# Kernel optimization log

Hardware: AMD Instinct MI355X
Metric: run time of the kernel (lower is better)

Reference implementation:

```python
import jax, jax.numpy as jnp
import numpy as np

B, C, H, W = 4, 64, 160, 160
OUT, KH, KW = 64, 3, 3
STRIDE, PAD = 1, 1
K2 = KH * KW


def conv2d(x, w, b=None, stride=STRIDE, pad=PAD):
    y = jax.lax.conv_general_dilated(
        x, w, window_strides=(stride, stride),
        padding=[(pad, pad), (pad, pad)],
        dimension_numbers=("NCHW", "OIHW", "NCHW"))
    if b is not None:
        y = y + b[None, :, None, None]
    return y


def bilinear_gather(x, py, px):
    # x: [B,C,H,W]; py,px: [B,K2,Ho,Wo] float sampling positions
    Bq, Cq, Hq, Wq = x.shape
    y0 = jnp.floor(py)
    x0 = jnp.floor(px)
    wy1 = py - y0  # frac
    wx1 = px - x0
    y0i = y0.astype(jnp.int32)
    x0i = x0.astype(jnp.int32)
    x_flat = x.reshape(Bq, Cq, Hq * Wq)

    def corner(yi, xi, wgt):
        valid = (yi >= 0) & (yi < Hq) & (xi >= 0) & (xi < Wq)
        idx = jnp.clip(yi, 0, Hq - 1) * Wq + jnp.clip(xi, 0, Wq - 1)  # [B,K2,Ho,Wo]
        g = jax.vmap(lambda xf, i: jnp.take(xf, i, axis=1))(x_flat, idx)  # [B,C,K2,Ho,Wo]
        return g * (wgt * valid)[:, None]

    out = corner(y0i, x0i, (1 - wy1) * (1 - wx1))
    out = out + corner(y0i, x0i + 1, (1 - wy1) * wx1)
    out = out + corner(y0i + 1, x0i, wy1 * (1 - wx1))
    out = out + corner(y0i + 1, x0i + 1, wy1 * wx1)
    return out  # [B,C,K2,Ho,Wo]


def deform_forward(x, offset_w, offset_b, mask_w, mask_b, dcn_w):
    offset = conv2d(x, offset_w, offset_b)                # [B, 2*K2, Ho, Wo]
    mask = jax.nn.sigmoid(conv2d(x, mask_w, mask_b))      # [B, K2, Ho, Wo]
    Bq, _, Ho, Wo = offset.shape
    off = offset.reshape(Bq, K2, 2, Ho, Wo)
    off_y, off_x = off[:, :, 0], off[:, :, 1]
    k = jnp.arange(K2)
    ky = (k // KW).astype(jnp.float32)
    kx = (k % KW).astype(jnp.float32)
    base_i = jnp.arange(Ho, dtype=jnp.float32) * STRIDE - PAD
    base_j = jnp.arange(Wo, dtype=jnp.float32) * STRIDE - PAD
    py = off_y + base_i[None, None, :, None] + ky[None, :, None, None]
    px = off_x + base_j[None, None, None, :] + kx[None, :, None, None]
    sampled = bilinear_gather(x, py, px)                  # [B,C,K2,Ho,Wo]
    w = dcn_w.reshape(OUT, C, K2)
    # out[b,o,i,j] = sum_{c,k} w[o,c,k] * mask[b,k,i,j] * sampled[b,c,k,i,j]
    return jnp.einsum("ock,bckij,bkij->boij", w, sampled, mask)


def setup_inputs() -> dict:
    key = jax.random.key(0)
    ks = jax.random.split(key, 6)
    x = jax.random.normal(ks[0], (B, C, H, W), dtype=jnp.float32)
    # small random weights so offsets stay modest (module inits them to 0;
    # random values exercise the full deformable math)
    offset_w = jax.random.normal(ks[1], (2 * K2, C, KH, KW), dtype=jnp.float32) * 0.01
    offset_b = jax.random.normal(ks[2], (2 * K2,), dtype=jnp.float32) * 0.1
    mask_w = jax.random.normal(ks[3], (K2, C, KH, KW), dtype=jnp.float32) * 0.01
    mask_b = jax.random.normal(ks[4], (K2,), dtype=jnp.float32) * 0.1
    dcn_w = jax.random.normal(ks[5], (OUT, C, KH, KW), dtype=jnp.float32) * (1.0 / np.sqrt(C * K2))
    return {"x": x, "offset_w": offset_w, "offset_b": offset_b,
            "mask_w": mask_w, "mask_b": mask_b, "dcn_w": dcn_w}


def reference(x, offset_w, offset_b, mask_w, mask_b, dcn_w):
    return deform_forward(x, offset_w, offset_b, mask_w, mask_b, dcn_w)
```

## Files before the change

kernel.cpp:

```cpp
#include <hip/hip_runtime.h>
#include <math.h>

#define Bq 4
#define Cq 64
#define Hq 160
#define Wq 160
#define HWq (Hq*Wq)
#define OUTq 64
#define KKq 576
#define KS  18
#define SROW 584
#define HSTRIDE 72

typedef __attribute__((ext_vector_type(8))) _Float16 half8;
typedef __attribute__((ext_vector_type(2))) _Float16 half2v;
typedef __attribute__((ext_vector_type(4))) float float4v;
typedef __attribute__((ext_vector_type(4))) unsigned short ushort4v;
typedef unsigned short ushort_t;
typedef unsigned int uint_t;

__device__ __forceinline__ ushort_t f2h(float f) {
    return __builtin_bit_cast(ushort_t, (_Float16)f);
}
__device__ __forceinline__ uint_t f2hdup(float f) {
    uint_t u = (uint_t)f2h(f);
    return u | (u << 16);
}
__device__ __forceinline__ half2v h2(uint_t u) {
    return __builtin_bit_cast(half2v, u);
}
#define MFMA16(a,b,c) __builtin_amdgcn_mfma_f32_16x16x32_f16((a),(b),(c),0,0,0)

__global__ void __launch_bounds__(256) k_prep(const float* __restrict__ x,
                                              const float* __restrict__ dcn_w,
                                              const float* __restrict__ off_w,
                                              const float* __restrict__ msk_w,
                                              ushort_t* __restrict__ xt,
                                              ushort_t* __restrict__ wtf,
                                              ushort_t* __restrict__ cwf2) {
    __shared__ float tile[64][65];
    int b = blockIdx.y, hw0 = blockIdx.x * 64;
    int tid = threadIdx.x;
    int l16 = tid & 15, crow = tid >> 4;
#pragma unroll
    for (int i = 0; i < 4; ++i) {
        int c = crow + i*16;
        float4 v = *(const float4*)(x + ((size_t)(b*Cq + c))*HWq + hw0 + l16*4);
        tile[c][l16*4+0] = v.x;
        tile[c][l16*4+1] = v.y;
        tile[c][l16*4+2] = v.z;
        tile[c][l16*4+3] = v.w;
    }
    __syncthreads();
#pragma unroll
    for (int it = 0; it < 4; ++it) {
        int hw = (tid >> 4) + it*16;
        int c4 = (tid & 15) * 4;
        uint_t v0 = (uint_t)f2h(tile[c4+0][hw]) | ((uint_t)f2h(tile[c4+1][hw]) << 16);
        uint_t v1 = (uint_t)f2h(tile[c4+2][hw]) | ((uint_t)f2h(tile[c4+3][hw]) << 16);
        uint2 vv; vv.x = v0; vv.y = v1;
        *(uint2*)(xt + ((size_t)b*HWq + hw0 + hw)*64 + c4) = vv;
    }
    if (blockIdx.y == 0 && blockIdx.x < 216) {
        int id = blockIdx.x*256 + tid;
        if (id < 4*KS*512) {
            int j = id & 7, ln = (id>>3) & 63, ks = (id>>9) % KS, g = id/(512*KS);
            int kk = ks*32 + (ln>>4)*8 + j;
            int c  = kk & 63, kt = kk >> 6;
            int m  = g*16 + (ln&15);
            wtf[id] = f2h(dcn_w[m*KKq + c*9 + kt]);
        }
        int id2 = id - 4*KS*512;
        if (id2 >= 0 && id2 < 9*2*2*512) {
            int j = id2 & 7, ln = (id2>>3) & 63;
            int ks2 = (id2>>9) & 1, g = (id2>>10) & 1, k = id2 >> 11;
            int co = g*16 + (ln&15);
            int c  = ks2*32 + (ln>>4)*8 + j;
            float w = 0.f;
            if (co < 18)      w = off_w[co*KKq + c*9 + k];
            else if (co < 27) w = msk_w[(co-18)*KKq + c*9 + k];
            cwf2[id2] = f2h(w);
        }
    }
}

__global__ void __launch_bounds__(256, 7) k_fused(const ushort_t* __restrict__ xt,
                                                  const ushort_t* __restrict__ cwf2,
                                                  const float* __restrict__ off_b,
                                                  const float* __restrict__ msk_b,
                                                  const ushort_t* __restrict__ wtf,
                                                  float* __restrict__ out) {
    __shared__ __align__(16) char s_mem[16*SROW*2];
    __shared__ __align__(16) ushort4v s_A16[144];
    __shared__ __align__(16) uint4 s_W[144];
    ushort_t* halo   = (ushort_t*)s_mem;
    float*    s_part = (float*)(s_mem + 7776);
    ushort_t* s_s    = (ushort_t*)s_mem;

    int blk = blockIdx.x;
    int jt = blk % 10, i = (blk/10) % Hq, b = blk/(10*Hq);
    int j0 = jt*16;
    int tid = threadIdx.x, lane = tid & 63, grp = tid >> 6;
    int n = lane & 15, quad = lane >> 4;

    const ushort_t* xtb = xt + (size_t)b*HWq*64;
    for (int t = tid; t < 432; t += 256) {
        int seg = t >> 3, sub = t & 7;
        int ky = seg / 18, px = seg % 18;
        int y = i + ky - 1, xx = j0 + px - 1;
        uint4 v = {0u,0u,0u,0u};
        if (y >= 0 && y < Hq && xx >= 0 && xx < Wq)
            v = *(const uint4*)(xtb + ((size_t)y*Wq + xx)*64 + sub*8);
        *(uint4*)(halo + (ky*18 + px)*HSTRIDE + sub*8) = v;
    }
    __syncthreads();

    {
        int gM = grp & 1, kh = grp >> 1;
        float4v cacc = {0.f,0.f,0.f,0.f};
#pragma unroll
        for (int s = 0; s < 9; ++s) {
            int st = kh*9 + s;
            int k = st >> 1, ks2 = st & 1;
            int ky = k/3, kx = k - (k/3)*3;
            half8 a  = *(const half8*)(cwf2 + (size_t)(((k*2+gM)*2+ks2)*512 + lane*8));
            half8 bf = *(const half8*)(halo + (ky*18 + n + kx)*HSTRIDE + quad*8 + ks2*32);
            cacc = MFMA16(a, bf, cacc);
        }
        *(float4v*)(s_part + grp*256 + lane*4) = cacc;
    }
    __syncthreads();

    if (tid < 144) {
        int p = tid & 15, k = tid >> 4;
        #define RD(co) (s_part[(((co)>>4)*256)     + ((((co)&15)>>2)*16 + p)*4 + ((co)&3)] + \
                        s_part[(2 + ((co)>>4))*256 + ((((co)&15)>>2)*16 + p)*4 + ((co)&3)])
        float oy = RD(2*k)   + off_b[2*k];
        float ox = RD(2*k+1) + off_b[2*k+1];
        float mv = RD(18+k)  + msk_b[k];
        #undef RD
        float m = 1.f/(1.f + __expf(-mv));
        float py = oy + (float)(i - 1 + k/3);
        float px = ox + (float)(j0 + p - 1 + (k - (k/3)*3));
        float fy = floorf(py), fx = floorf(px);
        int y0 = (int)fy, x0 = (int)fx;
        float wy1 = py - fy, wx1 = px - fx;
        float wy0 = 1.f - wy1, wx0 = 1.f - wx1;
        bool vy0 = (y0 >= 0) & (y0 < Hq),   vy1 = (y0+1 >= 0) & (y0+1 < Hq);
        bool vx0 = (x0 >= 0) & (x0 < Wq),   vx1 = (x0+1 >= 0) & (x0+1 < Wq);
        int yc0 = min(max(y0,   0), Hq-1), yc1 = min(max(y0+1, 0), Hq-1);
        int xc0 = min(max(x0,   0), Wq-1), xc1 = min(max(x0+1, 0), Wq-1);
        ushort4v av;
        av.x = (ushort_t)(yc0*Wq + xc0);
        av.y = (ushort_t)(yc0*Wq + xc1);
        av.z = (ushort_t)(yc1*Wq + xc0);
        av.w = (ushort_t)(yc1*Wq + xc1);
        s_A16[tid] = av;
        s_W[tid] = make_uint4(f2hdup((vy0 && vx0) ? wy0*wx0*m : 0.f),
                              f2hdup((vy0 && vx1) ? wy0*wx1*m : 0.f),
                              f2hdup((vy1 && vx0) ? wy1*wx0*m : 0.f),
                              f2hdup((vy1 && vx1) ? wy1*wx1*m : 0.f));
    }
    __syncthreads();

    {
        int lane4 = (lane & 31) * 4;
        int halfi = lane >> 5;
        const char* xtbB = (const char*)xtb;
        char* s_sb = (char*)s_s;
#pragma unroll 2
        for (int iter = 0; iter < 18; ++iter) {
            int t2h = iter*8 + grp*2 + halfi;
            ushort4v A = s_A16[t2h];
            uint4 Wt   = s_W[t2h];
            uint_t dst = (uint_t)((t2h & 15)*(SROW*2) + (t2h >> 4)*128);
            uint_t u00 = *(const uint_t*)(xtbB + (((uint_t)A.x) << 7) + lane4);
            uint_t u01 = *(const uint_t*)(xtbB + (((uint_t)A.y) << 7) + lane4);
            uint_t u10 = *(const uint_t*)(xtbB + (((uint_t)A.z) << 7) + lane4);
            uint_t u11 = *(const uint_t*)(xtbB + (((uint_t)A.w) << 7) + lane4);
            half2v acc2 = h2(u00) * h2(Wt.x);
            acc2 = __builtin_elementwise_fma(h2(u01), h2(Wt.y), acc2);
            acc2 = __builtin_elementwise_fma(h2(u10), h2(Wt.z), acc2);
            acc2 = __builtin_elementwise_fma(h2(u11), h2(Wt.w), acc2);
            *(uint_t*)(s_sb + dst + lane4) = __builtin_bit_cast(uint_t, acc2);
        }
    }
    __syncthreads();

    float4v acc = {0.f,0.f,0.f,0.f};
    const ushort_t* arow = wtf + ((size_t)(grp*KS)*64 + lane)*8;
    const ushort_t* brow = s_s + n*SROW + quad*8;
#pragma unroll
    for (int ks = 0; ks < KS; ++ks) {
        half8 a  = *(const half8*)(arow + ks*512);
        half8 bf = *(const half8*)(brow + ks*32);
        acc = MFMA16(a, bf, acc);
    }

#pragma unroll
    for (int r = 0; r < 4; ++r) {
        int o = grp*16 + quad*4 + r;
        out[(((size_t)b*OUTq + o)*Hq + i)*Wq + j0 + n] = acc[r];
    }
}

extern "C" void kernel_launch(void* const* d_in, const int* in_sizes, int n_in,
                              void* d_out, int out_size, void* d_ws, size_t ws_size,
                              hipStream_t stream) {
    const float* x     = (const float*)d_in[0];
    const float* off_w = (const float*)d_in[1];
    const float* off_b = (const float*)d_in[2];
    const float* msk_w = (const float*)d_in[3];
    const float* msk_b = (const float*)d_in[4];
    const float* dcn_w = (const float*)d_in[5];
    float* out = (float*)d_out;

    char* ws = (char*)d_ws;
    ushort_t* xt   = (ushort_t*)ws;
    ushort_t* wtf  = xt + (size_t)Bq*HWq*64;
    ushort_t* cwf2 = wtf + 4*KS*512;

    hipLaunchKernelGGL(k_prep, dim3(HWq/64, Bq), dim3(256), 0, stream,
                       x, dcn_w, off_w, msk_w, xt, wtf, cwf2);
    hipLaunchKernelGGL(k_fused, dim3(Bq*Hq*10), dim3(256), 0, stream,
                       xt, cwf2, off_b, msk_b, wtf, out);
}
```

Baseline: 133.4 us.

## Widen halo tile and serve bilinear gathers from LDS when in range

The halo loaded into shared memory grows from 3x18 to 5x20 pixels and now has its own buffer instead of sharing space with the sample matrix. The bilinear sampling phase encodes each corner as a halo-relative LDS byte offset when all four corners fall inside the tile. Otherwise it sets a flag bit and falls back to global gathers. This aims to replace most scattered global loads with LDS reads, since offsets are usually small. In exchange, shared memory use grows, the launch-bounds occupancy hint drops from 7 to 4, and half-waves may diverge between the two paths.

```diff
diff --git a/kernel.cpp b/kernel.cpp
--- a/kernel.cpp
+++ b/kernel.cpp
@@ -11,6 +11,9 @@
 #define KS  18
 #define SROW 584
 #define HSTRIDE 72
+#define HROWPX 20
+#define HROWS  5
+#define HALO_B (HROWS*HROWPX*HSTRIDE*2)
 
 typedef __attribute__((ext_vector_type(8))) _Float16 half8;
 typedef __attribute__((ext_vector_type(2))) _Float16 half2v;
@@ -84,18 +87,18 @@
     }
 }
 
-__global__ void __launch_bounds__(256, 7) k_fused(const ushort_t* __restrict__ xt,
+__global__ void __launch_bounds__(256, 4) k_fused(const ushort_t* __restrict__ xt,
                                                   const ushort_t* __restrict__ cwf2,
                                                   const float* __restrict__ off_b,
                                                   const float* __restrict__ msk_b,
                                                   const ushort_t* __restrict__ wtf,
                                                   float* __restrict__ out) {
-    __shared__ __align__(16) char s_mem[16*SROW*2];
+    __shared__ __align__(16) char s_mem[HALO_B + 16*SROW*2];
     __shared__ __align__(16) ushort4v s_A16[144];
     __shared__ __align__(16) uint4 s_W[144];
     ushort_t* halo   = (ushort_t*)s_mem;
-    float*    s_part = (float*)(s_mem + 7776);
-    ushort_t* s_s    = (ushort_t*)s_mem;
+    float*    s_part = (float*)(s_mem + HALO_B);
+    ushort_t* s_s    = (ushort_t*)(s_mem + HALO_B);
 
     int blk = blockIdx.x;
     int jt = blk % 10, i = (blk/10) % Hq, b = blk/(10*Hq);
@@ -104,14 +107,14 @@
     int n = lane & 15, quad = lane >> 4;
 
     const ushort_t* xtb = xt + (size_t)b*HWq*64;
-    for (int t = tid; t < 432; t += 256) {
+    for (int t = tid; t < HROWS*HROWPX*8; t += 256) {
         int seg = t >> 3, sub = t & 7;
-        int ky = seg / 18, px = seg % 18;
-        int y = i + ky - 1, xx = j0 + px - 1;
+        int r = seg / HROWPX, px = seg % HROWPX;
+        int y = i + r - 2, xx = j0 + px - 2;
         uint4 v = {0u,0u,0u,0u};
-        if (y >= 0 && y < Hq && xx >= 0 && xx < Wq)
+        if ((unsigned)y < (unsigned)Hq && (unsigned)xx < (unsigned)Wq)
             v = *(const uint4*)(xtb + ((size_t)y*Wq + xx)*64 + sub*8);
-        *(uint4*)(halo + (ky*18 + px)*HSTRIDE + sub*8) = v;
+        *(uint4*)(halo + (r*HROWPX + px)*HSTRIDE + sub*8) = v;
     }
     __syncthreads();
 
@@ -124,7 +127,7 @@
             int k = st >> 1, ks2 = st & 1;
             int ky = k/3, kx = k - (k/3)*3;
             half8 a  = *(const half8*)(cwf2 + (size_t)(((k*2+gM)*2+ks2)*512 + lane*8));
-            half8 bf = *(const half8*)(halo + (ky*18 + n + kx)*HSTRIDE + quad*8 + ks2*32);
+            half8 bf = *(const half8*)(halo + ((ky+1)*HROWPX + (n + kx + 1))*HSTRIDE + quad*8 + ks2*32);
             cacc = MFMA16(a, bf, cacc);
         }
         *(float4v*)(s_part + grp*256 + lane*4) = cacc;
@@ -151,10 +154,22 @@
         int yc0 = min(max(y0,   0), Hq-1), yc1 = min(max(y0+1, 0), Hq-1);
         int xc0 = min(max(x0,   0), Wq-1), xc1 = min(max(x0+1, 0), Wq-1);
         ushort4v av;
-        av.x = (ushort_t)(yc0*Wq + xc0);
-        av.y = (ushort_t)(yc0*Wq + xc1);
-        av.z = (ushort_t)(yc1*Wq + xc0);
-        av.w = (ushort_t)(yc1*Wq + xc1);
+        bool inh = (yc0 >= i-2) && (yc1 <= i+2) && (xc0 >= j0-2) && (xc1 <= j0+17);
+        if (inh) {
+            int ry0 = (yc0 - (i-2)) * (HROWPX*HSTRIDE*2);
+            int ry1 = (yc1 - (i-2)) * (HROWPX*HSTRIDE*2);
+            int cx0 = (xc0 - (j0-2)) * (HSTRIDE*2);
+            int cx1 = (xc1 - (j0-2)) * (HSTRIDE*2);
+            av.x = (ushort_t)(ry0 + cx0);
+            av.y = (ushort_t)(ry0 + cx1);
+            av.z = (ushort_t)(ry1 + cx0);
+            av.w = (ushort_t)(ry1 + cx1);
+        } else {
+            av.x = (ushort_t)((yc0*Wq + xc0) | 0x8000);
+            av.y = (ushort_t)((yc0*Wq + xc1) | 0x8000);
+            av.z = (ushort_t)((yc1*Wq + xc0) | 0x8000);
+            av.w = (ushort_t)((yc1*Wq + xc1) | 0x8000);
+        }
         s_A16[tid] = av;
         s_W[tid] = make_uint4(f2hdup((vy0 && vx0) ? wy0*wx0*m : 0.f),
                               f2hdup((vy0 && vx1) ? wy0*wx1*m : 0.f),
@@ -167,17 +182,28 @@
         int lane4 = (lane & 31) * 4;
         int halfi = lane >> 5;
         const char* xtbB = (const char*)xtb;
+        const char* haloB = (const char*)s_mem;
         char* s_sb = (char*)s_s;
 #pragma unroll 2
         for (int iter = 0; iter < 18; ++iter) {
             int t2h = iter*8 + grp*2 + halfi;
-            ushort4v A = s_A16[t2h];
-            uint4 Wt   = s_W[t2h];
+            uint2 Ad = *(const uint2*)(&s_A16[t2h]);
+            uint4 Wt = s_W[t2h];
+            uint_t a0 = Ad.x & 0xffffu, a1 = Ad.x >> 16;
+            uint_t a2 = Ad.y & 0xffffu, a3 = Ad.y >> 16;
             uint_t dst = (uint_t)((t2h & 15)*(SROW*2) + (t2h >> 4)*128);
-            uint_t u00 = *(const uint_t*)(xtbB + (((uint_t)A.x) << 7) + lane4);
-            uint_t u01 = *(const uint_t*)(xtbB + (((uint_t)A.y) << 7) + lane4);
-            uint_t u10 = *(const uint_t*)(xtbB + (((uint_t)A.z) << 7) + lane4);
-            uint_t u11 = *(const uint_t*)(xtbB + (((uint_t)A.w) << 7) + lane4);
+            uint_t u00, u01, u10, u11;
+            if (a0 < 0x8000u) {
+                u00 = *(const uint_t*)(haloB + a0 + lane4);
+                u01 = *(const uint_t*)(haloB + a1 + lane4);
+                u10 = *(const uint_t*)(haloB + a2 + lane4);
+                u11 = *(const uint_t*)(haloB + a3 + lane4);
+            } else {
+                u00 = *(const uint_t*)(xtbB + ((a0 & 0x7fffu) << 7) + lane4);
+                u01 = *(const uint_t*)(xtbB + ((a1 & 0x7fffu) << 7) + lane4);
+                u10 = *(const uint_t*)(xtbB + ((a2 & 0x7fffu) << 7) + lane4);
+                u11 = *(const uint_t*)(xtbB + ((a3 & 0x7fffu) << 7) + lane4);
+            }
             half2v acc2 = h2(u00) * h2(Wt.x);
             acc2 = __builtin_elementwise_fma(h2(u01), h2(Wt.y), acc2);
             acc2 = __builtin_elementwise_fma(h2(u10), h2(Wt.z), acc2);
```

Result: slower. 139.9 us (+4.9%).
